# Kernel tuning notes

Measured on AMD Instinct MI355X. Metric: run time of the kernel, lower is better.

Reference implementation:

```python
import jax, jax.numpy as jnp
import numpy as np

DIM = 1024
N_HEAD = 16
DIM_HEAD = DIM // N_HEAD
B, L = 4, 2048


def setup_inputs() -> dict:
    key = jax.random.key(0)
    k1, k2, k3, k4, k5 = jax.random.split(key, 5)
    scale = 1.0 / np.sqrt(DIM)
    return {
        "x": jax.random.normal(k1, (B, L, DIM), dtype=jnp.float32),
        "qkv_w": jax.random.normal(k2, (3 * DIM, DIM), dtype=jnp.float32) * scale,
        "qkv_b": jax.random.normal(k3, (3 * DIM,), dtype=jnp.float32) * 0.02,
        "out_w": jax.random.normal(k4, (DIM, DIM), dtype=jnp.float32) * scale,
        "out_b": jax.random.normal(k5, (DIM,), dtype=jnp.float32) * 0.02,
    }


def reference(x, qkv_w, qkv_b, out_w, out_b):
    batch, length, dim = x.shape
    # qkv projection: torch Linear is x @ W.T + b
    qkv = x @ qkv_w.T + qkv_b  # [B, L, 3*dim]
    qkv = qkv.reshape(batch, length, 3, N_HEAD, DIM_HEAD)
    qkv = jnp.transpose(qkv, (2, 0, 3, 1, 4))  # [3, B, H, L, Dh]
    q, k, v = qkv[0], qkv[1], qkv[2]
    attn = jnp.einsum("bhqd,bhkd->bhqk", q, k) / jnp.sqrt(jnp.float32(DIM_HEAD))
    attn = jax.nn.softmax(attn, axis=-1)  # dropout=0 -> identity
    out = jnp.einsum("bhqk,bhkd->bhqd", attn, v)  # [B, H, L, Dh]
    out = jnp.transpose(out, (0, 2, 1, 3)).reshape(batch, length, dim)
    return out @ out_w.T + out_b
```

## Files before the change

kernel.cpp:

```cpp
#include <hip/hip_runtime.h>
#include <math.h>
#include <stdint.h>

typedef __bf16 bf16;
typedef __bf16 bf16x4 __attribute__((ext_vector_type(4)));
typedef __bf16 bf16x8 __attribute__((ext_vector_type(8)));
typedef float f32x4 __attribute__((ext_vector_type(4)));

#define DIMT 1024
#define NH 16
#define DH 64
#define BATCH 4
#define SEQ 2048
#define M_TOT (BATCH*SEQ)

#define SCQ 0.18033688011112042f

__global__ void detect_kernel(const uint16_t* __restrict__ xbits, int* flag) {
    __shared__ int cnt;
    if (threadIdx.x == 0) cnt = 0;
    __syncthreads();
    int local = 0;
    for (int i = threadIdx.x; i < 16384; i += 256) {
        const uint16_t v = xbits[i];
        if ((v & 0x7F80) == 0x7F80) local++;
    }
    atomicAdd(&cnt, local);
    __syncthreads();
    if (threadIdx.x == 0) *flag = (cnt > 0) ? 1 : 0;
}

#define V8_X   1048576L
#define V8_WQ  393216L
#define V8_BQ  384L
#define V8_WO  131072L
#define V8_BO  128L
#define V8_C0  (V8_X)
#define V8_C1  (V8_C0 + V8_WQ)
#define V8_C2  (V8_C1 + V8_BQ)
#define V8_C3  (V8_C2 + V8_WO)
#define V8_TOT (V8_C3 + V8_BO)

__global__ void cvt_all_kernel(const void* __restrict__ s0, const void* __restrict__ s1,
                               const void* __restrict__ s2, const void* __restrict__ s3,
                               const void* __restrict__ s4,
                               bf16* __restrict__ dst, const int* __restrict__ flag) {
    const bool f32 = (*flag != 0);
    const long stride = (long)gridDim.x * blockDim.x;
    for (long v = (long)blockIdx.x * blockDim.x + threadIdx.x; v < V8_TOT; v += stride) {
        const void* src; long off;
        if (v < V8_C0)      { src = s0; off = v; }
        else if (v < V8_C1) { src = s1; off = v - V8_C0; }
        else if (v < V8_C2) { src = s2; off = v - V8_C1; }
        else if (v < V8_C3) { src = s3; off = v - V8_C2; }
        else                { src = s4; off = v - V8_C3; }
        if (f32) {
            const float4 a = ((const float4*)src)[off * 2];
            const float4 b = ((const float4*)src)[off * 2 + 1];
            bf16x8 r;
            r[0] = (bf16)a.x; r[1] = (bf16)a.y; r[2] = (bf16)a.z; r[3] = (bf16)a.w;
            r[4] = (bf16)b.x; r[5] = (bf16)b.y; r[6] = (bf16)b.z; r[7] = (bf16)b.w;
            *(bf16x8*)(dst + v * 8) = r;
        } else {
            *(bf16x8*)(dst + v * 8) = ((const bf16x8*)src)[off];
        }
    }
}

template<bool QKV>
__global__ __launch_bounds__(256) void gemm_nt_128(
    const bf16* __restrict__ A, const bf16* __restrict__ W,
    const bf16* __restrict__ bias,
    float* __restrict__ CoutF, bf16* __restrict__ CoutH,
    const int* __restrict__ flag,
    int N, int K,
    bf16* __restrict__ Qo, bf16* __restrict__ Ko, bf16* __restrict__ Vo)
{
    __shared__ __align__(16) bf16 As[128 * 64];
    __shared__ __align__(16) bf16 Bs[128 * 64];

    const int tid = threadIdx.x;
    const int w = tid >> 6, lane = tid & 63;
    const int lane15 = lane & 15, quad = lane >> 4;
    const int wr = w >> 1, wc = w & 1;

    const int lin = blockIdx.y * gridDim.x + blockIdx.x;
    const int xcd = lin & 7;
    const int j5 = lin >> 3;
    const int m0 = (xcd * 8 + (j5 & 7)) * 128;
    const int n0 = (j5 >> 3) * 128;

    const int rs = lane >> 3;
    const int c8sw = (lane & 7) ^ rs;
    const bf16* ag[4]; const bf16* wg[4]; int lo[4];
    #pragma unroll
    for (int j = 0; j < 4; j++) {
        const int s = j * 4 + w;
        ag[j] = A + (long)(m0 + s * 8 + rs) * K + c8sw * 8;
        wg[j] = W + (long)(n0 + s * 8 + rs) * K + c8sw * 8;
        lo[j] = s * 512 + lane * 8;
    }

    const int r7 = lane15 & 7;
    int abase[4], bbase[4];
    #pragma unroll
    for (int i = 0; i < 4; i++) {
        abase[i] = ((wr * 8 + i * 2) + (lane15 >> 3)) * 512 + r7 * 64;
        bbase[i] = ((wc * 8 + i * 2) + (lane15 >> 3)) * 512 + r7 * 64;
    }

    f32x4 acc[4][4] = {};
    for (int k0 = 0; k0 < K; k0 += 64) {
        __syncthreads();
        #pragma unroll
        for (int j = 0; j < 4; j++) {
            __builtin_amdgcn_global_load_lds(
                (const __attribute__((address_space(1))) void*)(ag[j] + k0),
                (__attribute__((address_space(3))) void*)(As + lo[j]), 16, 0, 0);
            __builtin_amdgcn_global_load_lds(
                (const __attribute__((address_space(1))) void*)(wg[j] + k0),
                (__attribute__((address_space(3))) void*)(Bs + lo[j]), 16, 0, 0);
        }
        __syncthreads();

        #pragma unroll
        for (int ks = 0; ks < 2; ks++) {
            bf16x8 af[4], bfr[4];
            #pragma unroll
            for (int i = 0; i < 4; i++)
                af[i] = *(const bf16x8*)&As[abase[i] + (((ks * 4 + quad) ^ r7) * 8)];
            #pragma unroll
            for (int i = 0; i < 4; i++)
                bfr[i] = *(const bf16x8*)&Bs[bbase[i] + (((ks * 4 + quad) ^ r7) * 8)];
            #pragma unroll
            for (int i = 0; i < 4; i++)
                #pragma unroll
                for (int jj = 0; jj < 4; jj++)
                    acc[i][jj] = __builtin_amdgcn_mfma_f32_16x16x32_bf16(af[i], bfr[jj], acc[i][jj], 0, 0, 0);
        }
    }

    const bool f32out = QKV ? false : (*flag != 0);
    const bool vblock = QKV && (n0 >= 2 * DIMT);

    #pragma unroll
    for (int i = 0; i < 4; i++)
    #pragma unroll
    for (int jj = 0; jj < 4; jj++) {
        const int colg = n0 + wc * 64 + jj * 16 + lane15;
        const float bb = (float)bias[colg];
        const int rbase = m0 + wr * 64 + i * 16 + quad * 4;
        if (QKV && vblock) {
            const int rem = colg & 1023;
            const int h = rem >> 6, dh = rem & 63;
            const int b = rbase >> 11, l = rbase & 2047;
            const int bh = b * NH + h;
            bf16x4 pv;
            #pragma unroll
            for (int r = 0; r < 4; r++) pv[r] = (bf16)(acc[i][jj][r] + bb);
            *(bf16x4*)&Vo[((long)bh * DH + dh) * SEQ + l] = pv;
        } else {
            #pragma unroll
            for (int r = 0; r < 4; r++) {
                const int rowg = rbase + r;
                float val = acc[i][jj][r] + bb;
                if (QKV) {
                    const int which = colg >> 10;
                    const int rem = colg & 1023;
                    const int h = rem >> 6, dh = rem & 63;
                    const int b = rowg >> 11, l = rowg & 2047;
                    if (which == 0) val *= SCQ;
                    bf16* dst = (which == 0) ? Qo : Ko;
                    dst[(((long)(b * NH + h)) * SEQ + l) * DH + dh] = (bf16)val;
                } else {
                    const long idx = (long)rowg * N + colg;
                    if (f32out) CoutF[idx] = val;
                    else        CoutH[idx] = (bf16)val;
                }
            }
        }
    }
}

__global__ __launch_bounds__(512, 4) void attn_kernel(
    const bf16* __restrict__ Q, const bf16* __restrict__ K,
    const bf16* __restrict__ V, bf16* __restrict__ O)
{
    __shared__ __align__(16) bf16 Ks[2][64 * 64];
    __shared__ __align__(16) bf16 Vts[2][64 * 64];
    __shared__ __align__(16) bf16 Pst[8][32][72];

    const int tid = threadIdx.x;
    const int wave = tid >> 6, lane = tid & 63;
    const int lane15 = lane & 15, quad = lane >> 4;
    const int bh = blockIdx.x;
    const int b = bh >> 4, h = bh & 15;
    const int q0 = blockIdx.y * 256;

    const bf16* Qb = Q + (long)bh * SEQ * DH;
    const bf16* Kb = K + (long)bh * SEQ * DH;
    const bf16* Vb = V + (long)bh * DH * SEQ;

    bf16x8 qf[2][2];
    #pragma unroll
    for (int ms = 0; ms < 2; ms++) {
        const long qr = q0 + wave * 32 + ms * 16 + lane15;
        qf[ms][0] = *(const bf16x8*)(Qb + qr * DH + quad * 8);
        qf[ms][1] = *(const bf16x8*)(Qb + qr * DH + 32 + quad * 8);
    }

    bf16x8 ones;
    #pragma unroll
    for (int e = 0; e < 8; e++) ones[e] = (bf16)1.0f;

    f32x4 o_acc[2][4] = {};
    f32x4 o_l[2] = {};

    const int l8 = lane >> 3, l7b = lane & 7;
    const int c8sw = l7b ^ l8;
    const int srow = wave * 8 + l8;
    const int ldso = wave * 512 + lane * 8;
    const bf16* kgp = Kb + (long)srow * DH + c8sw * 8;
    const bf16* vgp = Vb + (long)srow * SEQ + c8sw * 8;

    const int r7 = lane15 & 7;

    auto STAGE = [&](int kt, int bi) {
        __builtin_amdgcn_global_load_lds(
            (const __attribute__((address_space(1))) void*)(kgp + (long)kt * (64 * DH)),
            (__attribute__((address_space(3))) void*)(&Ks[bi][ldso]), 16, 0, 0);
        __builtin_amdgcn_global_load_lds(
            (const __attribute__((address_space(1))) void*)(vgp + kt * 64),
            (__attribute__((address_space(3))) void*)(&Vts[bi][ldso]), 16, 0, 0);
    };

    auto TILE = [&](const bf16* KsB, const bf16* VtB) {
        f32x4 sT[2][4];
        #pragma unroll
        for (int kn = 0; kn < 4; kn++) {
            const int krow = kn * 16 + lane15;
            bf16x8 k0 = *(const bf16x8*)&KsB[krow * 64 + ((quad ^ r7) * 8)];
            bf16x8 k1 = *(const bf16x8*)&KsB[krow * 64 + (((4 + quad) ^ r7) * 8)];
            #pragma unroll
            for (int ms = 0; ms < 2; ms++) {
                f32x4 a = {};
                a = __builtin_amdgcn_mfma_f32_16x16x32_bf16(k0, qf[ms][0], a, 0, 0, 0);
                a = __builtin_amdgcn_mfma_f32_16x16x32_bf16(k1, qf[ms][1], a, 0, 0, 0);
                sT[ms][kn] = a;
            }
        }

        #pragma unroll
        for (int ms = 0; ms < 2; ms++)
            #pragma unroll
            for (int kn = 0; kn < 4; kn++) {
                bf16x4 p4;
                #pragma unroll
                for (int r = 0; r < 4; r++)
                    p4[r] = (bf16)__builtin_amdgcn_exp2f(sT[ms][kn][r]);
                *(bf16x4*)&Pst[wave][ms * 16 + lane15][kn * 16 + quad * 4] = p4;
            }

        bf16x8 pf[2][2];
        #pragma unroll
        for (int ms = 0; ms < 2; ms++) {
            pf[ms][0] = *(const bf16x8*)&Pst[wave][ms * 16 + lane15][quad * 8];
            pf[ms][1] = *(const bf16x8*)&Pst[wave][ms * 16 + lane15][32 + quad * 8];
            o_l[ms] = __builtin_amdgcn_mfma_f32_16x16x32_bf16(pf[ms][0], ones, o_l[ms], 0, 0, 0);
            o_l[ms] = __builtin_amdgcn_mfma_f32_16x16x32_bf16(pf[ms][1], ones, o_l[ms], 0, 0, 0);
        }

        #pragma unroll
        for (int dn = 0; dn < 4; dn++) {
            const int vrow = dn * 16 + lane15;
            bf16x8 vf0 = *(const bf16x8*)&VtB[vrow * 64 + ((quad ^ r7) * 8)];
            bf16x8 vf1 = *(const bf16x8*)&VtB[vrow * 64 + (((4 + quad) ^ r7) * 8)];
            #pragma unroll
            for (int ms = 0; ms < 2; ms++) {
                o_acc[ms][dn] = __builtin_amdgcn_mfma_f32_16x16x32_bf16(pf[ms][0], vf0, o_acc[ms][dn], 0, 0, 0);
                o_acc[ms][dn] = __builtin_amdgcn_mfma_f32_16x16x32_bf16(pf[ms][1], vf1, o_acc[ms][dn], 0, 0, 0);
            }
        }
    };

    STAGE(0, 0);
    __syncthreads();
    for (int kt = 0; kt < SEQ / 64; kt += 2) {
        STAGE(kt + 1, 1);
        TILE(&Ks[0][0], &Vts[0][0]);
        __syncthreads();
        if (kt + 2 < SEQ / 64) STAGE(kt + 2, 0);
        TILE(&Ks[1][0], &Vts[1][0]);
        __syncthreads();
    }

    #pragma unroll
    for (int ms = 0; ms < 2; ms++) {
        float rcl[4];
        #pragma unroll
        for (int r = 0; r < 4; r++) rcl[r] = 1.0f / o_l[ms][r];
        #pragma unroll
        for (int dn = 0; dn < 4; dn++)
            #pragma unroll
            for (int r = 0; r < 4; r++) {
                const int rowl = q0 + wave * 32 + ms * 16 + quad * 4 + r;
                const int col = h * DH + dn * 16 + lane15;
                O[((long)b * SEQ + rowl) * DIMT + col] = (bf16)(o_acc[ms][dn][r] * rcl[r]);
            }
    }
}

extern "C" void kernel_launch(void* const* d_in, const int* in_sizes, int n_in,
                              void* d_out, int out_size, void* d_ws, size_t ws_size,
                              hipStream_t stream) {
    const void* x     = d_in[0];
    const void* qkv_w = d_in[1];
    const void* qkv_b = d_in[2];
    const void* out_w = d_in[3];
    const void* out_b = d_in[4];

    const long n_x  = (long)M_TOT * DIMT;
    const long n_wq = 3L * DIMT * DIMT;
    const long n_bq = 3L * DIMT;
    const long n_wo = (long)DIMT * DIMT;
    const long n_bo = DIMT;

    int* flag = (int*)d_ws;
    bf16* xb = (bf16*)((char*)d_ws + 64);
    bf16* wq = xb + n_x;
    bf16* bq = wq + n_wq;
    bf16* wo = bq + n_bq;
    bf16* bo = wo + n_wo;
    bf16* qb = bo + n_bo;
    bf16* kb = qb + n_x;
    bf16* vb = kb + n_x;
    bf16* ob = vb + n_x;

    detect_kernel<<<1, 256, 0, stream>>>((const uint16_t*)x, flag);
    cvt_all_kernel<<<2048, 256, 0, stream>>>(x, qkv_w, qkv_b, out_w, out_b, xb, flag);

    dim3 g1(3 * DIMT / 128, M_TOT / 128);
    gemm_nt_128<true><<<g1, 256, 0, stream>>>(xb, wq, bq,
                                              (float*)nullptr, (bf16*)nullptr, flag,
                                              3 * DIMT, DIMT, qb, kb, vb);

    dim3 g2(BATCH * NH, SEQ / 256);
    attn_kernel<<<g2, 512, 0, stream>>>(qb, kb, vb, ob);

    dim3 g3(DIMT / 128, M_TOT / 128);
    gemm_nt_128<false><<<g3, 256, 0, stream>>>(ob, wo, bo,
                                               (float*)d_out, (bf16*)d_out, flag,
                                               DIMT, DIMT, qb, kb, vb);
}
```

Before: 285.6 us.

## Use 256x128 tiled QKV GEMM with 512 threads and raise attention MFMA priority

Replaces the 128x128 QKV projection GEMM with a dedicated 256x128 tile kernel run by 8 waves. Each B tile is reused across more rows, and the kernel uses an XCD-aware block mapping. The epilogue writes Q/K scattered and V transposed as before. It also wraps the attention TILE compute in s_setprio to favour MFMA-issuing waves. The larger tile needs more LDS and registers, which may reduce occupancy, and the single-buffered loop still syncs twice per k-step.

```diff
diff --git a/kernel.cpp b/kernel.cpp
--- a/kernel.cpp
+++ b/kernel.cpp
@@ -67,6 +67,111 @@
     }
 }
 
+__global__ __launch_bounds__(512, 6) void gemm_qkv_256(
+    const bf16* __restrict__ A, const bf16* __restrict__ W,
+    const bf16* __restrict__ bias, int K,
+    bf16* __restrict__ Qo, bf16* __restrict__ Ko, bf16* __restrict__ Vo)
+{
+    __shared__ __align__(16) bf16 As[256 * 64];
+    __shared__ __align__(16) bf16 Bs[128 * 64];
+
+    const int tid = threadIdx.x;
+    const int w = tid >> 6, lane = tid & 63;
+    const int lane15 = lane & 15, quad = lane >> 4;
+    const int wr = w >> 1, wc = w & 1;
+
+    const int lin = blockIdx.y * gridDim.x + blockIdx.x;
+    const int xcd = lin & 7;
+    const int j5 = lin >> 3;
+    const int m0 = (xcd * 4 + (j5 & 3)) * 256;
+    const int n0 = (j5 >> 2) * 128;
+
+    const int trow = tid >> 3, t7 = tid & 7;
+    const int csw = t7 ^ (trow & 7);
+    const bf16* ag[4]; const bf16* wg[2];
+    #pragma unroll
+    for (int j = 0; j < 4; j++)
+        ag[j] = A + (long)(m0 + j * 64 + trow) * K + csw * 8;
+    #pragma unroll
+    for (int j = 0; j < 2; j++)
+        wg[j] = W + (long)(n0 + j * 64 + trow) * K + csw * 8;
+    const int lo = tid * 8;
+
+    const int r7 = lane15 & 7;
+    int abase[4], bbase[4];
+    #pragma unroll
+    for (int i = 0; i < 4; i++) {
+        abase[i] = ((wr * 8 + i * 2) + (lane15 >> 3)) * 512 + r7 * 64;
+        bbase[i] = ((wc * 8 + i * 2) + (lane15 >> 3)) * 512 + r7 * 64;
+    }
+
+    f32x4 acc[4][4] = {};
+    for (int k0 = 0; k0 < K; k0 += 64) {
+        __syncthreads();
+        #pragma unroll
+        for (int j = 0; j < 4; j++)
+            __builtin_amdgcn_global_load_lds(
+                (const __attribute__((address_space(1))) void*)(ag[j] + k0),
+                (__attribute__((address_space(3))) void*)(As + j * 4096 + lo), 16, 0, 0);
+        #pragma unroll
+        for (int j = 0; j < 2; j++)
+            __builtin_amdgcn_global_load_lds(
+                (const __attribute__((address_space(1))) void*)(wg[j] + k0),
+                (__attribute__((address_space(3))) void*)(Bs + j * 4096 + lo), 16, 0, 0);
+        __syncthreads();
+
+        #pragma unroll
+        for (int ks = 0; ks < 2; ks++) {
+            bf16x8 af[4], bfr[4];
+            #pragma unroll
+            for (int i = 0; i < 4; i++)
+                af[i] = *(const bf16x8*)&As[abase[i] + (((ks * 4 + quad) ^ r7) * 8)];
+            #pragma unroll
+            for (int i = 0; i < 4; i++)
+                bfr[i] = *(const bf16x8*)&Bs[bbase[i] + (((ks * 4 + quad) ^ r7) * 8)];
+            #pragma unroll
+            for (int i = 0; i < 4; i++)
+                #pragma unroll
+                for (int jj = 0; jj < 4; jj++)
+                    acc[i][jj] = __builtin_amdgcn_mfma_f32_16x16x32_bf16(af[i], bfr[jj], acc[i][jj], 0, 0, 0);
+        }
+    }
+
+    const bool vblock = (n0 >= 2 * DIMT);
+
+    #pragma unroll
+    for (int i = 0; i < 4; i++)
+    #pragma unroll
+    for (int jj = 0; jj < 4; jj++) {
+        const int colg = n0 + wc * 64 + jj * 16 + lane15;
+        const float bb = (float)bias[colg];
+        const int rbase = m0 + wr * 64 + i * 16 + quad * 4;
+        if (vblock) {
+            const int rem = colg & 1023;
+            const int h = rem >> 6, dh = rem & 63;
+            const int b = rbase >> 11, l = rbase & 2047;
+            const int bh = b * NH + h;
+            bf16x4 pv;
+            #pragma unroll
+            for (int r = 0; r < 4; r++) pv[r] = (bf16)(acc[i][jj][r] + bb);
+            *(bf16x4*)&Vo[((long)bh * DH + dh) * SEQ + l] = pv;
+        } else {
+            #pragma unroll
+            for (int r = 0; r < 4; r++) {
+                const int rowg = rbase + r;
+                float val = acc[i][jj][r] + bb;
+                const int which = colg >> 10;
+                const int rem = colg & 1023;
+                const int h = rem >> 6, dh = rem & 63;
+                const int b = rowg >> 11, l = rowg & 2047;
+                if (which == 0) val *= SCQ;
+                bf16* dst = (which == 0) ? Qo : Ko;
+                dst[(((long)(b * NH + h)) * SEQ + l) * DH + dh] = (bf16)val;
+            }
+        }
+    }
+}
+
 template<bool QKV>
 __global__ __launch_bounds__(256) void gemm_nt_128(
     const bf16* __restrict__ A, const bf16* __restrict__ W,
@@ -235,6 +340,7 @@
     };
 
     auto TILE = [&](const bf16* KsB, const bf16* VtB) {
+        __builtin_amdgcn_s_setprio(1);
         f32x4 sT[2][4];
         #pragma unroll
         for (int kn = 0; kn < 4; kn++) {
@@ -281,6 +387,7 @@
                 o_acc[ms][dn] = __builtin_amdgcn_mfma_f32_16x16x32_bf16(pf[ms][1], vf1, o_acc[ms][dn], 0, 0, 0);
             }
         }
+        __builtin_amdgcn_s_setprio(0);
     };
 
     STAGE(0, 0);
@@ -339,10 +446,8 @@
     detect_kernel<<<1, 256, 0, stream>>>((const uint16_t*)x, flag);
     cvt_all_kernel<<<2048, 256, 0, stream>>>(x, qkv_w, qkv_b, out_w, out_b, xb, flag);
 
-    dim3 g1(3 * DIMT / 128, M_TOT / 128);
-    gemm_nt_128<true><<<g1, 256, 0, stream>>>(xb, wq, bq,
-                                              (float*)nullptr, (bf16*)nullptr, flag,
-                                              3 * DIMT, DIMT, qb, kb, vb);
+    dim3 g1(3 * DIMT / 128, M_TOT / 256);
+    gemm_qkv_256<<<g1, 512, 0, stream>>>(xb, wq, bq, DIMT, qb, kb, vb);
 
     dim3 g2(BATCH * NH, SEQ / 256);
     attn_kernel<<<g2, 512, 0, stream>>>(qb, kb, vb, ob);
```

Result: slower. 529.9 us (+85.5%).
